# Kernel optimization log

Measured on AMD Instinct MI355X. Metric: run time of the kernel, lower is better.

Reference implementation:

```python
import jax, jax.numpy as jnp
import numpy as np

NUM_CLASSES = 80
ALPHA = 1.0
BETA = 6.0
EPS = 1e-9      # assigner eps
IOU_EPS = 1e-7  # bbox_iou eps


def _iou_xyxy(b1, b2):
    # b1: (B, A, 1, 4), b2: (B, 1, M, 4) -> IoU (B, A, M); matches bbox_iou(xywh=False)
    b1x1, b1y1, b1x2, b1y2 = (b1[..., 0], b1[..., 1], b1[..., 2], b1[..., 3])
    b2x1, b2y1, b2x2, b2y2 = (b2[..., 0], b2[..., 1], b2[..., 2], b2[..., 3])
    w1, h1 = b1x2 - b1x1, b1y2 - b1y1 + IOU_EPS
    w2, h2 = b2x2 - b2x1, b2y2 - b2y1 + IOU_EPS
    iw = jnp.clip(jnp.minimum(b1x2, b2x2) - jnp.maximum(b1x1, b2x1), 0)
    ih = jnp.clip(jnp.minimum(b1y2, b2y2) - jnp.maximum(b1y1, b2y1), 0)
    inter = iw * ih
    union = w1 * h1 + w2 * h2 - inter + IOU_EPS
    return inter / union


def _select_highest_overlaps(mask_pos, overlaps, M):
    # Always apply the dedup branch; it is a no-op when no anchor has >1 gt.
    fg = mask_pos.sum(-1)                                   # (B, A)
    multi = fg > 1
    is_max = jax.nn.one_hot(overlaps.argmax(-1), M, dtype=mask_pos.dtype)  # (B, A, M)
    mask_pos = jnp.where(multi[..., None], is_max, mask_pos)
    fg = mask_pos.sum(-1)
    tgt = mask_pos.argmax(-1).astype(jnp.int32)             # (B, A)
    return tgt, fg, mask_pos


def _forward(pd_scores, pd_bboxes, anc_points, gt_labels, gt_bboxes, mask_gt):
    B, A, C = pd_scores.shape
    M = gt_bboxes.shape[1]
    f = pd_scores.dtype
    mgt_b = mask_gt.astype(bool)                            # (B, M)
    mgt_f = mask_gt.astype(f)

    # --- box metrics ---
    overlaps = jnp.clip(_iou_xyxy(pd_bboxes[:, :, None, :], gt_bboxes[:, None, :, :]), 0)  # (B,A,M)
    idx = jnp.broadcast_to(gt_labels[:, None, :].astype(jnp.int32), (B, A, M))
    cls_scores = jnp.take_along_axis(pd_scores, idx, axis=-1)                              # (B,A,M)
    align_metric = cls_scores ** ALPHA * overlaps ** BETA

    # --- anchors inside gt boxes ---
    lt = anc_points[None, :, None, :] - gt_bboxes[:, None, :, :2]   # (B,A,M,2)
    rb = gt_bboxes[:, None, :, 2:] - anc_points[None, :, None, :]
    mask_in_gts = jnp.concatenate([lt, rb], -1).min(-1) > EPS       # (B,A,M) bool
    mask_pos = mask_in_gts.astype(f) * mgt_f[:, None, :]

    # --- fix 1 (vectorized: each (b,gt) iteration only touches its own column) ---
    need1 = mgt_b & (mask_pos.sum(1) == 0)                          # (B,M)
    has_in = mask_in_gts.any(1)                                     # (B,M)
    best1 = jnp.where(has_in, (overlaps * mask_in_gts).argmax(1), overlaps.argmax(1))  # (B,M)
    oh1 = jax.nn.one_hot(best1, A, dtype=f).transpose(0, 2, 1)      # (B,A,M)
    mask_pos = jnp.maximum(mask_pos, oh1 * need1[:, None, :].astype(f))

    tgt, fg, mask_pos = _select_highest_overlaps(mask_pos, overlaps, M)

    # --- fix 2: sequential per-gt reassignment (order-dependent -> lax.scan) ---
    anchor_ids = jnp.arange(A)
    gt_ids = jnp.arange(M)

    def step(carry, g):
        mp, tgi, fgm = carry
        assigned = jnp.any((fgm > 0) & (tgi == g), axis=1)          # (B,)
        need = jnp.take(mgt_b, g, axis=1) & (~assigned)             # (B,)
        best = jnp.take(overlaps, g, axis=2).argmax(1)              # (B,)
        oh_b = anchor_ids[None, :] == best[:, None]                 # (B,A) bool
        upd = need[:, None] & oh_b                                  # (B,A)
        col = (gt_ids == g)[None, None, :]
        mp = jnp.where(upd[:, :, None] & col, jnp.asarray(1, mp.dtype), mp)
        tgi = jnp.where(upd, g, tgi)
        fgm = jnp.where(upd, jnp.asarray(1, fgm.dtype), fgm)
        return (mp, tgi, fgm), None

    (mask_pos, tgt, fg), _ = jax.lax.scan(step, (mask_pos, tgt, fg), jnp.arange(M, dtype=jnp.int32))
    tgt, fg, mask_pos = _select_highest_overlaps(mask_pos, overlaps, M)

    # --- targets ---
    tl = jnp.take_along_axis(gt_labels.astype(jnp.int32), tgt, axis=1)   # (B,A)
    tl = jnp.clip(tl, 0, NUM_CLASSES)
    tb = jnp.take_along_axis(gt_bboxes, tgt[..., None], axis=1)          # (B,A,4)
    ts = jax.nn.one_hot(tl, C, dtype=f)                                  # (B,A,C)
    ts = jnp.where(fg[..., None] > 0, ts, jnp.asarray(0, f))

    # --- normalize scores by task-aligned metric ---
    am = align_metric * mask_pos
    pam = am.max(-1, keepdims=True)                                      # (B,A,1)
    pov = (overlaps * mask_pos).max(-1, keepdims=True)
    norm = (am * pov / (pam + EPS)).max(-1, keepdims=True)               # (B,A,1)
    ts = ts * norm
    return tl, tb, ts, fg > 0, tgt


def setup_inputs() -> dict:
    key = jax.random.key(0)
    B, C, M, IMG = 32, NUM_CLASSES, 32, 640
    ks = jax.random.split(key, 8)
    # YOLO-style anchor grid: strides 8/16/32 -> 80^2 + 40^2 + 20^2 = 8400 points
    pts = []
    for s in (8, 16, 32):
        n = IMG // s
        xs = (np.arange(n, dtype=np.float32) + 0.5) * s
        gy, gx = np.meshgrid(xs, xs, indexing="ij")
        pts.append(np.stack([gx.ravel(), gy.ravel()], -1))
    anc_points = jnp.asarray(np.concatenate(pts, 0))                     # (8400, 2)
    A = anc_points.shape[0]
    pd_scores = jax.random.uniform(ks[0], (B, A, C), dtype=jnp.float32)  # sigmoid-like scores
    wh_p = jax.random.uniform(ks[1], (B, A, 2), minval=16.0, maxval=256.0)
    ctr_p = anc_points[None] + jax.random.normal(ks[2], (B, A, 2)) * 8.0
    pd_bboxes = jnp.concatenate([ctr_p - wh_p / 2, ctr_p + wh_p / 2], -1)
    ctr_g = jax.random.uniform(ks[3], (B, M, 2), minval=60.0, maxval=580.0)
    wh_g = jax.random.uniform(ks[4], (B, M, 2), minval=24.0, maxval=240.0)
    gt_bboxes = jnp.concatenate([ctr_g - wh_g / 2, ctr_g + wh_g / 2], -1)
    gt_labels = jax.random.randint(ks[5], (B, M), 0, C, dtype=jnp.int32)
    n_gt = jax.random.randint(ks[6], (B, 1), 1, M + 1)
    mask_gt = jnp.arange(M)[None, :] < n_gt                              # (B, M) bool
    return dict(pd_scores=pd_scores, pd_bboxes=pd_bboxes, anc_points=anc_points,
                gt_labels=gt_labels, gt_bboxes=gt_bboxes, mask_gt=mask_gt)


def reference(pd_scores, pd_bboxes, anc_points, gt_labels, gt_bboxes, mask_gt):
    return _forward(pd_scores, pd_bboxes, anc_points, gt_labels, gt_bboxes, mask_gt)
```

## Files before the change

kernel.cpp:

```cpp
#include <hip/hip_runtime.h>


#define EPS_IN   1e-9f
#define IOU_EPS  1e-7f

__device__ __forceinline__ float iou_pair(const float4 p, const float4 g) {
#pragma clang fp contract(off)
    float w1 = p.z - p.x;
    float h1 = (p.w - p.y) + IOU_EPS;
    float w2 = g.z - g.x;
    float h2 = (g.w - g.y) + IOU_EPS;
    float iw = fminf(p.z, g.z) - fmaxf(p.x, g.x);
    iw = fmaxf(iw, 0.0f);
    float ih = fminf(p.w, g.w) - fmaxf(p.y, g.y);
    ih = fmaxf(ih, 0.0f);
    float inter = iw * ih;
    float uni = w1 * h1 + w2 * h2 - inter + IOU_EPS;
    float r = inter / uni;
    return fmaxf(r, 0.0f);
}

__device__ __forceinline__ int detect_mode(const void* mg, int nw) {
    const unsigned* w = (const unsigned*)mg;
    int lane = threadIdx.x & 63;
    int badI = 0, badF = 0;
    for (int i = lane; i < nw; i += 64) {
        unsigned v = w[i];
        badI |= (v > 1u);
        badF |= (v != 0u && v != 0x3F800000u);
    }
    unsigned long long bI = __ballot(badI != 0);
    unsigned long long bF = __ballot(badF != 0);
    return bI ? (bF ? 2 : 1) : 0;
}

__device__ __forceinline__ bool mask_at(const void* mg, int mode, int idx) {
    if (mode == 0) return ((const int*)mg)[idx] != 0;
    if (mode == 1) return ((const float*)mg)[idx] != 0.0f;
    return ((const unsigned char*)mg)[idx] != 0;
}

__global__ void k_phase1(const float4* __restrict__ pdb, const float2* __restrict__ anc,
                         const float4* __restrict__ gtb, const void* mg, int nw,
                         unsigned long long* __restrict__ colKey,
                         unsigned char* __restrict__ needByte,
                         unsigned* __restrict__ rowbits0, short* __restrict__ tgt0,
                         int* __restrict__ cntChunk,
                         int A, int M, int nCh) {
    int b = blockIdx.y, tid = threadIdx.x;
    int mode = detect_mode(mg, nw);
    size_t bA = (size_t)b * A;

    if ((int)blockIdx.x < M) {
        int m = blockIdx.x;
        if (!mask_at(mg, mode, b * M + m)) return;
        float4 g = gtb[b * M + m];
        unsigned long long key = 0ull;
        int hasin = 0;
        for (int a = tid; a < A; a += 256) {
            float v = iou_pair(pdb[bA + a], g);
            unsigned long long k =
                ((unsigned long long)__float_as_uint(v) << 32) | (0xFFFFFFFFu - (unsigned)a);
            if (k > key) key = k;
            float2 an = anc[a];
            float mn = fminf(fminf(an.x - g.x, an.y - g.y), fminf(g.z - an.x, g.w - an.y));
            hasin |= (mn > EPS_IN);
        }
        __shared__ unsigned long long skey[4];
        __shared__ int sin_[4];
        int lane = tid & 63, wid = tid >> 6;
        for (int off = 32; off; off >>= 1) {
            unsigned long long o = __shfl_down(key, off);
            if (o > key) key = o;
            hasin |= __shfl_down(hasin, off);
        }
        if (lane == 0) { skey[wid] = key; sin_[wid] = hasin; }
        __syncthreads();
        if (tid == 0) {
            for (int i = 1; i < 4; i++) { if (skey[i] > key) key = skey[i]; hasin |= sin_[i]; }
            colKey[b * M + m] = key;
            needByte[b * M + m] = hasin ? 0 : 1;
        }
    } else {
        int ch = blockIdx.x - M;
        int a = ch * 256 + tid;
        __shared__ float4 sg[32];
        __shared__ unsigned char smg[32];
        __shared__ int shist[32];
        if (tid < M) {
            sg[tid]  = gtb[b * M + tid];
            smg[tid] = mask_at(mg, mode, b * M + tid) ? 1 : 0;
        }
        if (tid < 32) shist[tid] = 0;
        __syncthreads();
        if (a < A) {
            float2 an = anc[a];
            unsigned bits = 0u;
            for (int m = 0; m < M; m++) {
                float4 g = sg[m];
                float mn = fminf(fminf(an.x - g.x, an.y - g.y), fminf(g.z - an.x, g.w - an.y));
                if (mn > EPS_IN && smg[m]) bits |= (1u << m);
            }
            rowbits0[bA + a] = bits;
            int pc = __popc(bits);
            int t;
            if (pc > 1) {
                float4 p = pdb[bA + a];
                float bv = -1.0f; int bm = 0;
                for (int m = 0; m < M; m++) {
                    float v = iou_pair(p, sg[m]);
                    if (v > bv) { bv = v; bm = m; }
                }
                t = bm;
            } else if (pc == 1) t = __ffs(bits) - 1;
            else t = -1;
            tgt0[bA + a] = (short)t;
            if (t >= 0) atomicAdd(&shist[t], 1);
        }
        __syncthreads();
        if (tid < 32) cntChunk[((size_t)b * nCh + ch) * 32 + tid] = shist[tid];
    }
}

__global__ void k_final(const float* __restrict__ pds, const float4* __restrict__ pdb,
                        const float4* __restrict__ gtb, const int* __restrict__ gtl,
                        const void* mg, int nw,
                        const unsigned long long* __restrict__ colKey,
                        const unsigned char* __restrict__ needByte,
                        const unsigned* __restrict__ rowbits0,
                        const short* __restrict__ tgt0,
                        const int* __restrict__ cntChunk,
                        float* __restrict__ out,
                        int A, int M, int C, int B, int nCh) {
    int b = blockIdx.y;
    int base = blockIdx.x * 256;
    int tid = threadIdx.x;
    int mode = detect_mode(mg, nw);
    size_t bA = (size_t)b * A;
    __shared__ float4 sg[32];
    __shared__ int slab[32];
    __shared__ int ovrA[64];
    __shared__ unsigned ovrAdd[64];
    __shared__ short ovrT[64];
    __shared__ int sNov;
    __shared__ float snorm[256];
    __shared__ int stl[256];
    if (tid < 32) {
        sg[tid]   = (tid < M) ? gtb[b * M + tid] : make_float4(0.f, 0.f, 0.f, 0.f);
        slab[tid] = (tid < M) ? gtl[b * M + tid] : 0;
    }
    __syncthreads();

    if (tid < 64) {
        bool mv = false, needv = false;
        int best = -1, c0 = 0;
        if (tid < M) mv = mask_at(mg, mode, b * M + tid);
        if (mv) {
            unsigned long long key = colKey[b * M + tid];
            best = (int)(0xFFFFFFFFu - (unsigned)(key & 0xFFFFFFFFull));
            needv = (needByte[b * M + tid] != 0);
        }
        if (tid < 32) {
            for (int ch = 0; ch < nCh; ch++)
                c0 += cntChunk[((size_t)b * nCh + ch) * 32 + tid];
        }
        int myPre = (mv && best >= 0) ? (int)tgt0[bA + best] : -1;
        unsigned maskbits = (unsigned)__ballot(mv);
        unsigned needBits = (unsigned)__ballot(needv);
        unsigned myEq = 0u;
        for (int g2 = 0; g2 < 32; g2++) {
            int bb = __shfl(best, g2);
            if (bb == best) myEq |= (1u << g2);
        }
        int nov = 0;
        unsigned rem = needBits;
        while (rem) {
            int gl = __ffs(rem) - 1;
            unsigned em = __shfl(myEq, gl) & needBits;
            rem &= ~em;
            int aF = __shfl(best, gl);
            unsigned addb = em;
            unsigned bits1 = rowbits0[bA + aF] | addb;
            int t1;
            if (__popc(bits1) > 1) {
                float4 p = pdb[bA + aF];
                unsigned long long kk = 0ull;
                if (tid < M) {
                    float vv = iou_pair(p, sg[tid]);
                    kk = ((unsigned long long)__float_as_uint(vv) << 32) |
                         (0xFFFFFFFFu - (unsigned)tid);
                }
                for (int off = 32; off; off >>= 1) {
                    unsigned long long o = __shfl_down(kk, off);
                    if (o > kk) kk = o;
                }
                kk = __shfl(kk, 0);
                t1 = (int)(0xFFFFFFFFu - (unsigned)(kk & 0xFFFFFFFFull));
            } else {
                t1 = __ffs(bits1) - 1;
            }
            int t0a = __shfl(myPre, gl);
            if (tid == t0a && t0a >= 0) c0--;
            if (tid == t1) c0++;
            if (best == aF) myPre = t1;
            if (tid == 0) { ovrA[nov] = aF; ovrAdd[nov] = addb; }
            nov++;
        }
        unsigned applied = 0u;
        for (int g = 0; g < M; g++) {
            int cg = __shfl(c0, g);
            if (((maskbits >> g) & 1u) && cg == 0) {
                int aa      = __shfl(best, g);
                unsigned em = __shfl(myEq, g);
                unsigned x  = applied & em;
                int old;
                if (x) old = 31 - __clz(x);
                else   old = __shfl(myPre, g);
                if (tid == old) c0--;
                if (tid == g)   c0++;
                applied |= (1u << g);
                if (tid == 0) { ovrA[nov] = aa; ovrAdd[nov] = 1u << g; }
                nov++;
            }
        }
        if (tid == 0) sNov = nov;
    }
    __syncthreads();
    if (tid < 64) {
        int nov2 = sNov;
        for (int j = 0; j < nov2; j++) {
            int aj = ovrA[j];
            unsigned addT = 0u;
            for (int k = 0; k < nov2; k++) if (ovrA[k] == aj) addT |= ovrAdd[k];
            unsigned bt = rowbits0[bA + aj] | addT;
            int tf;
            if (__popc(bt) > 1) {
                float4 p = pdb[bA + aj];
                unsigned long long kk = 0ull;
                if (tid < M) {
                    float vv = iou_pair(p, sg[tid]);
                    kk = ((unsigned long long)__float_as_uint(vv) << 32) |
                         (0xFFFFFFFFu - (unsigned)tid);
                }
                for (int off = 32; off; off >>= 1) {
                    unsigned long long o = __shfl_down(kk, off);
                    if (o > kk) kk = o;
                }
                kk = __shfl(kk, 0);
                tf = (int)(0xFFFFFFFFu - (unsigned)(kk & 0xFFFFFFFFull));
            } else {
                tf = __ffs(bt) - 1;
            }
            if (tid == 0) ovrT[j] = (short)tf;
        }
    }
    __syncthreads();

    int a = base + tid;
    size_t BA = (size_t)B * A;
    if (a < A) {
        size_t idx = bA + a;
        int t = (int)tgt0[idx];
        int nov2 = sNov;
        for (int j = 0; j < nov2; j++)
            if (ovrA[j] == a) t = (int)ovrT[j];
        int fg = (t >= 0);
        int tgtO = fg ? t : 0;
        int lab = slab[tgtO];
        int tl = min(max(lab, 0), C);
        float norm = 0.0f;
        if (fg) {
            float ov = iou_pair(pdb[idx], sg[t]);
            int li = (lab >= 0 && lab < C) ? lab : 0;
            float cls = pds[idx * (size_t)C + li];
            float ov6 = powf(ov, 6.0f);
            float vv = cls * ov6;
            norm = vv * ov / (vv + 1e-9f);
        }
        out[idx] = (float)tl;
        ((float4*)(out + BA))[idx] = sg[tgtO];
        out[BA * (size_t)(5 + C) + idx] = fg ? 1.0f : 0.0f;
        out[BA * (size_t)(6 + C) + idx] = (float)tgtO;
        snorm[tid] = norm;
        stl[tid] = tl;
    }
    __syncthreads();
    int cntA = min(256, A - base);
    int rowf4 = C >> 2;
    int nf4 = cntA * rowf4;
    float4* tsb = (float4*)(out + BA * 5 + (bA + base) * C);
    int q = 256 / rowf4, r = 256 - q * rowf4;
    int row = tid / rowf4;
    int c4  = tid - row * rowf4;
    for (int i = tid; i < nf4; i += 256) {
        float nv = snorm[row];
        int tl   = stl[row];
        int cb = c4 * 4;
        float4 vv;
        vv.x = (tl == cb + 0) ? nv : 0.0f;
        vv.y = (tl == cb + 1) ? nv : 0.0f;
        vv.z = (tl == cb + 2) ? nv : 0.0f;
        vv.w = (tl == cb + 3) ? nv : 0.0f;
        tsb[i] = vv;
        row += q; c4 += r;
        if (c4 >= rowf4) { c4 -= rowf4; row++; }
    }
}

extern "C" void kernel_launch(void* const* d_in, const int* in_sizes, int n_in,
                              void* d_out, int out_size, void* d_ws, size_t ws_size,
                              hipStream_t stream) {
    const float*  pd_scores = (const float*)d_in[0];
    const float4* pd_bboxes = (const float4*)d_in[1];
    const float2* anc       = (const float2*)d_in[2];
    const int*    gt_labels = (const int*)d_in[3];
    const float4* gt_bboxes = (const float4*)d_in[4];
    const void*   mask_gt   = d_in[5];

    int A = in_sizes[2] / 2;
    int B = in_sizes[1] / (A * 4);
    int M = in_sizes[3] / B;
    int C = (int)((long long)in_sizes[0] / ((long long)B * A));
    int nCh = (A + 255) / 256;
    int nw = (B * M) / 4; if (nw > 256) nw = 256;

    char* wp = (char*)d_ws;
    auto carve = [&](size_t bytes) -> char* {
        char* r = wp; wp += (bytes + 255) & ~(size_t)255; return r;
    };
    unsigned* rowbits0         = (unsigned*)carve((size_t)B * A * 4);
    short* tgt0                = (short*)carve((size_t)B * A * 2);
    unsigned long long* colKey = (unsigned long long*)carve((size_t)B * M * 8);
    unsigned char* needByte    = (unsigned char*)carve((size_t)B * M);
    int* cntChunk              = (int*)carve((size_t)B * nCh * 32 * 4);

    float* out = (float*)d_out;

    k_phase1<<<dim3(M + nCh, B), 256, 0, stream>>>(pd_bboxes, anc, gt_bboxes, mask_gt, nw,
                                                   colKey, needByte, rowbits0, tgt0,
                                                   cntChunk, A, M, nCh);
    k_final<<<dim3(nCh, B), 256, 0, stream>>>(pd_scores, pd_bboxes, gt_bboxes, gt_labels,
                                              mask_gt, nw, colKey, needByte, rowbits0,
                                              tgt0, cntChunk, out, A, M, C, B, nCh);
}
```

Baseline: 51.78 us.

## Drop per-gt column blocks; compute column argmax lazily in final kernel

Phase 1 no longer launches one block per ground truth to scan every anchor for the best-IoU key and the has-inside flag. The has-inside flag now comes from a per-chunk OR of raw inside-box bits gathered during the anchor pass. The column argmax is recomputed inside each final block, and only for ground truths whose assigned count is at most M. The aim is to shorten phase 1 and remove its long-running column blocks. The cost is redundant full-anchor scans in every final block when any ground truth is flagged, and correctness rests on the count-based skip condition.

```diff
diff --git a/kernel.cpp b/kernel.cpp
--- a/kernel.cpp
+++ b/kernel.cpp
@@ -42,103 +42,80 @@
 
 __global__ void k_phase1(const float4* __restrict__ pdb, const float2* __restrict__ anc,
                          const float4* __restrict__ gtb, const void* mg, int nw,
-                         unsigned long long* __restrict__ colKey,
-                         unsigned char* __restrict__ needByte,
                          unsigned* __restrict__ rowbits0, short* __restrict__ tgt0,
-                         int* __restrict__ cntChunk,
+                         int* __restrict__ cntChunk, unsigned* __restrict__ hasinChunk,
                          int A, int M, int nCh) {
-    int b = blockIdx.y, tid = threadIdx.x;
+    int b = blockIdx.y, ch = blockIdx.x, tid = threadIdx.x;
+    int lane = tid & 63, wid = tid >> 6;
     int mode = detect_mode(mg, nw);
     size_t bA = (size_t)b * A;
-
-    if ((int)blockIdx.x < M) {
-        int m = blockIdx.x;
-        if (!mask_at(mg, mode, b * M + m)) return;
-        float4 g = gtb[b * M + m];
-        unsigned long long key = 0ull;
-        int hasin = 0;
-        for (int a = tid; a < A; a += 256) {
-            float v = iou_pair(pdb[bA + a], g);
-            unsigned long long k =
-                ((unsigned long long)__float_as_uint(v) << 32) | (0xFFFFFFFFu - (unsigned)a);
-            if (k > key) key = k;
-            float2 an = anc[a];
+    __shared__ float4 sg[32];
+    __shared__ unsigned char smg[32];
+    __shared__ int shist[32];
+    __shared__ unsigned sOr[4];
+    if (tid < 32) {
+        sg[tid]    = (tid < M) ? gtb[b * M + tid] : make_float4(0.f, 0.f, 0.f, 0.f);
+        smg[tid]   = (tid < M) && mask_at(mg, mode, b * M + tid) ? 1 : 0;
+        shist[tid] = 0;
+    }
+    __syncthreads();
+    int a = ch * 256 + tid;
+    unsigned inboxRaw = 0u, bits = 0u;
+    if (a < A) {
+        float2 an = anc[a];
+        for (int m = 0; m < M; m++) {
+            float4 g = sg[m];
             float mn = fminf(fminf(an.x - g.x, an.y - g.y), fminf(g.z - an.x, g.w - an.y));
-            hasin |= (mn > EPS_IN);
-        }
-        __shared__ unsigned long long skey[4];
-        __shared__ int sin_[4];
-        int lane = tid & 63, wid = tid >> 6;
-        for (int off = 32; off; off >>= 1) {
-            unsigned long long o = __shfl_down(key, off);
-            if (o > key) key = o;
-            hasin |= __shfl_down(hasin, off);
-        }
-        if (lane == 0) { skey[wid] = key; sin_[wid] = hasin; }
-        __syncthreads();
-        if (tid == 0) {
-            for (int i = 1; i < 4; i++) { if (skey[i] > key) key = skey[i]; hasin |= sin_[i]; }
-            colKey[b * M + m] = key;
-            needByte[b * M + m] = hasin ? 0 : 1;
-        }
-    } else {
-        int ch = blockIdx.x - M;
-        int a = ch * 256 + tid;
-        __shared__ float4 sg[32];
-        __shared__ unsigned char smg[32];
-        __shared__ int shist[32];
-        if (tid < M) {
-            sg[tid]  = gtb[b * M + tid];
-            smg[tid] = mask_at(mg, mode, b * M + tid) ? 1 : 0;
-        }
-        if (tid < 32) shist[tid] = 0;
-        __syncthreads();
-        if (a < A) {
-            float2 an = anc[a];
-            unsigned bits = 0u;
+            if (mn > EPS_IN) {
+                inboxRaw |= (1u << m);
+                if (smg[m]) bits |= (1u << m);
+            }
+        }
+        rowbits0[bA + a] = bits;
+        int pc = __popc(bits);
+        int t;
+        if (pc > 1) {
+            float4 p = pdb[bA + a];
+            float bv = -1.0f; int bm = 0;
             for (int m = 0; m < M; m++) {
-                float4 g = sg[m];
-                float mn = fminf(fminf(an.x - g.x, an.y - g.y), fminf(g.z - an.x, g.w - an.y));
-                if (mn > EPS_IN && smg[m]) bits |= (1u << m);
-            }
-            rowbits0[bA + a] = bits;
-            int pc = __popc(bits);
-            int t;
-            if (pc > 1) {
-                float4 p = pdb[bA + a];
-                float bv = -1.0f; int bm = 0;
-                for (int m = 0; m < M; m++) {
-                    float v = iou_pair(p, sg[m]);
-                    if (v > bv) { bv = v; bm = m; }
-                }
-                t = bm;
-            } else if (pc == 1) t = __ffs(bits) - 1;
-            else t = -1;
-            tgt0[bA + a] = (short)t;
-            if (t >= 0) atomicAdd(&shist[t], 1);
-        }
-        __syncthreads();
-        if (tid < 32) cntChunk[((size_t)b * nCh + ch) * 32 + tid] = shist[tid];
-    }
+                float v = iou_pair(p, sg[m]);
+                if (v > bv) { bv = v; bm = m; }
+            }
+            t = bm;
+        } else if (pc == 1) t = __ffs(bits) - 1;
+        else t = -1;
+        tgt0[bA + a] = (short)t;
+        if (t >= 0) atomicAdd(&shist[t], 1);
+    }
+    unsigned h = inboxRaw;
+    for (int off = 32; off; off >>= 1) h |= __shfl_xor(h, off);
+    if (lane == 0) sOr[wid] = h;
+    __syncthreads();
+    if (tid < 32) cntChunk[((size_t)b * nCh + ch) * 32 + tid] = shist[tid];
+    if (tid == 0) hasinChunk[b * nCh + ch] = sOr[0] | sOr[1] | sOr[2] | sOr[3];
 }
 
 __global__ void k_final(const float* __restrict__ pds, const float4* __restrict__ pdb,
                         const float4* __restrict__ gtb, const int* __restrict__ gtl,
                         const void* mg, int nw,
-                        const unsigned long long* __restrict__ colKey,
-                        const unsigned char* __restrict__ needByte,
                         const unsigned* __restrict__ rowbits0,
                         const short* __restrict__ tgt0,
                         const int* __restrict__ cntChunk,
+                        const unsigned* __restrict__ hasinChunk,
                         float* __restrict__ out,
                         int A, int M, int C, int B, int nCh) {
     int b = blockIdx.y;
     int base = blockIdx.x * 256;
     int tid = threadIdx.x;
+    int lane = tid & 63, wid = tid >> 6;
     int mode = detect_mode(mg, nw);
     size_t bA = (size_t)b * A;
     __shared__ float4 sg[32];
     __shared__ int slab[32];
+    __shared__ int sCnt0[32];
+    __shared__ unsigned long long sColKey[32];
+    __shared__ unsigned sFlagBits, sHorAll;
+    __shared__ unsigned long long sred[4];
     __shared__ int ovrA[64];
     __shared__ unsigned ovrAdd[64];
     __shared__ short ovrT[64];
@@ -152,19 +129,60 @@
     __syncthreads();
 
     if (tid < 64) {
-        bool mv = false, needv = false;
-        int best = -1, c0 = 0;
-        if (tid < M) mv = mask_at(mg, mode, b * M + tid);
-        if (mv) {
-            unsigned long long key = colKey[b * M + tid];
-            best = (int)(0xFFFFFFFFu - (unsigned)(key & 0xFFFFFFFFull));
-            needv = (needByte[b * M + tid] != 0);
-        }
+        unsigned h = 0u;
+        for (int ch = tid; ch < nCh; ch += 64) h |= hasinChunk[b * nCh + ch];
+        for (int off = 32; off; off >>= 1) h |= __shfl_xor(h, off);
+        int c0 = 0;
         if (tid < 32) {
             for (int ch = 0; ch < nCh; ch++)
                 c0 += cntChunk[((size_t)b * nCh + ch) * 32 + tid];
         }
-        int myPre = (mv && best >= 0) ? (int)tgt0[bA + best] : -1;
+        bool mv = (tid < M) && mask_at(mg, mode, b * M + tid);
+        bool flag = mv && (c0 <= M);
+        unsigned fb = (unsigned)__ballot(flag);
+        if (tid < 32) sCnt0[tid] = c0;
+        if (tid == 0) { sFlagBits = fb; sHorAll = h; }
+    }
+    __syncthreads();
+
+    unsigned fbits = sFlagBits;
+    while (fbits) {
+        int m = __ffs(fbits) - 1; fbits &= fbits - 1;
+        float4 gm = sg[m];
+        unsigned long long key = 0ull;
+        for (int aa = tid; aa < A; aa += 256) {
+            float vv = iou_pair(pdb[bA + aa], gm);
+            unsigned long long k2 =
+                ((unsigned long long)__float_as_uint(vv) << 32) |
+                (0xFFFFFFFFu - (unsigned)aa);
+            if (k2 > key) key = k2;
+        }
+        for (int off = 32; off; off >>= 1) {
+            unsigned long long o = __shfl_down(key, off);
+            if (o > key) key = o;
+        }
+        if (lane == 0) sred[wid] = key;
+        __syncthreads();
+        if (tid == 0) {
+            unsigned long long k3 = sred[0];
+            for (int i = 1; i < 4; i++) if (sred[i] > k3) k3 = sred[i];
+            sColKey[m] = k3;
+        }
+        __syncthreads();
+    }
+
+    if (tid < 64) {
+        unsigned flagBits = sFlagBits, horAll = sHorAll;
+        bool mv   = (tid < M) && mask_at(mg, mode, b * M + tid);
+        bool flag = (tid < 32) && ((flagBits >> tid) & 1u);
+        int best = -1;
+        if (flag) {
+            unsigned long long key = sColKey[tid];
+            best = (int)(0xFFFFFFFFu - (unsigned)(key & 0xFFFFFFFFull));
+        }
+        bool needv = mv && !((horAll >> tid) & 1u);
+        int c0 = (tid < 32) ? sCnt0[tid] : 0;
+        int myPre = (best >= 0) ? (int)tgt0[bA + best] : -1;
         unsigned maskbits = (unsigned)__ballot(mv);
         unsigned needBits = (unsigned)__ballot(needv);
         unsigned myEq = 0u;
@@ -328,18 +346,17 @@
     auto carve = [&](size_t bytes) -> char* {
         char* r = wp; wp += (bytes + 255) & ~(size_t)255; return r;
     };
-    unsigned* rowbits0         = (unsigned*)carve((size_t)B * A * 4);
-    short* tgt0                = (short*)carve((size_t)B * A * 2);
-    unsigned long long* colKey = (unsigned long long*)carve((size_t)B * M * 8);
-    unsigned char* needByte    = (unsigned char*)carve((size_t)B * M);
-    int* cntChunk              = (int*)carve((size_t)B * nCh * 32 * 4);
+    unsigned* rowbits0   = (unsigned*)carve((size_t)B * A * 4);
+    short* tgt0          = (short*)carve((size_t)B * A * 2);
+    int* cntChunk        = (int*)carve((size_t)B * nCh * 32 * 4);
+    unsigned* hasinChunk = (unsigned*)carve((size_t)B * nCh * 4);
 
     float* out = (float*)d_out;
 
-    k_phase1<<<dim3(M + nCh, B), 256, 0, stream>>>(pd_bboxes, anc, gt_bboxes, mask_gt, nw,
-                                                   colKey, needByte, rowbits0, tgt0,
-                                                   cntChunk, A, M, nCh);
+    k_phase1<<<dim3(nCh, B), 256, 0, stream>>>(pd_bboxes, anc, gt_bboxes, mask_gt, nw,
+                                               rowbits0, tgt0, cntChunk, hasinChunk,
+                                               A, M, nCh);
     k_final<<<dim3(nCh, B), 256, 0, stream>>>(pd_scores, pd_bboxes, gt_bboxes, gt_labels,
-                                              mask_gt, nw, colKey, needByte, rowbits0,
-                                              tgt0, cntChunk, out, A, M, C, B, nCh);
-}
+                                              mask_gt, nw, rowbits0, tgt0, cntChunk,
+                                              hasinChunk, out, A, M, C, B, nCh);
+}
```

New measurement: 94.33 us. 82.2% more time.
